# Kernel optimization log

Measured on AMD Instinct MI355X. Metric: run time of the kernel, lower is better.

## Reference

```python
import jax, jax.numpy as jnp
import numpy as np

B, HI, WI = 4, 24, 24
T = HI * WI
H, N = 12, 64
C = H * N
D_MIX, D_DECAY, D_AAA, D_KKK, D_GATE, D_MA, D_MK = 32, 64, 16, 16, 128, 16, 16


def q_shift(x, Hi, Wi):
    # 4-direction quarter-channel spatial shift (groups_q_shift, K=1, gamma=1/4)
    Bb, Nn, Cc = x.shape
    q = Cc // 4
    x4 = x.reshape(Bb, Hi, Wi, Cc)
    pad = lambda a, pw: jnp.pad(a, ((0, 0),) + pw + ((0, 0),))
    s1 = pad(x4[:, :, :-1, 0:q], ((0, 0), (1, 0)))        # shift right along W
    s2 = pad(x4[:, :, 1:, q:2 * q], ((0, 0), (0, 1)))     # shift left along W
    s3 = pad(x4[:, :-1, :, 2 * q:3 * q], ((1, 0), (0, 0)))  # shift down along H
    s4 = pad(x4[:, 1:, :, 3 * q:4 * q], ((0, 1), (0, 0)))   # shift up along H
    return jnp.concatenate([s1, s2, s3, s4], axis=-1).reshape(Bb, Nn, Cc)


def wkv7(r, w, k, v, a, b):
    # RWKV-7 delta-rule recurrence: S = S*diag(exp(w)) + S@(a b^T) + v k^T ; y = S r
    Bb, Tt, Cc = r.shape
    tohead = lambda t: t.reshape(Bb, Tt, H, N).transpose(1, 0, 2, 3)  # (T,B,H,N)
    rt, kt, vt, at, bt = map(tohead, (r, k, v, a, b))
    dt = jnp.exp(tohead(w))  # per-channel decay in (0, e^-0.5]

    def step(S, inp):
        r_, d_, k_, v_, a_, b_ = inp
        sa = jnp.einsum('bhij,bhj->bhi', S, a_)
        S = S * d_[:, :, None, :] + sa[..., None] * b_[:, :, None, :] + v_[..., None] * k_[:, :, None, :]
        return S, jnp.einsum('bhij,bhj->bhi', S, r_)

    S0 = jnp.zeros((Bb, H, N, N), r.dtype)
    _, ys = jax.lax.scan(step, S0, (rt, dt, kt, vt, at, bt))
    return ys.transpose(1, 0, 2, 3).reshape(Bb, Tt, Cc)


def group_norm(x, scale, bias, eps=64e-5):
    Bb, Tt, Cc = x.shape
    xg = x.reshape(Bb, Tt, H, N)
    mu = xg.mean(-1, keepdims=True)
    var = ((xg - mu) ** 2).mean(-1, keepdims=True)
    xn = ((xg - mu) * jax.lax.rsqrt(var + eps)).reshape(Bb, Tt, Cc)
    return xn * scale + bias


def fwd(x, maa_x, maa_rg, maa_wa, maa_k, maa_v, maa_w1, maa_w2,
        w0, wd1, wd2, a0, a1, a2, kk1, kk2, g1, g2,
        ma0, ma1, ma2, mk0, mk1, mk2, faaaa,
        Wr, Wk, Wv, Wo, ln_s, ln_b, h_img, w_img):
    Bb, Tt, Cc = x.shape
    xx = q_shift(x, h_img, w_img) - x
    xxx = x + xx * maa_x
    lora = jnp.tanh(xxx @ maa_w1).reshape(Bb, Tt, 4, D_MIX)
    m = jnp.einsum('btfd,fdc->fbtc', lora, maa_w2)  # (4,B,T,C)
    xrg = x + xx * (maa_rg + m[0])
    xwa = x + xx * (maa_wa + m[1])
    xk = x + xx * (maa_k + m[2])
    xv = x + xx * (maa_v + m[3])
    r = xrg @ Wr.T
    w = -jax.nn.softplus(-(w0 + jnp.tanh(xwa @ wd1) @ wd2)) - 0.5  # log-decay <= -0.5
    k = xk @ Wk.T
    v = xv @ Wv.T
    g = jax.nn.sigmoid(xrg @ g1) @ g2
    kk = k + jnp.tanh(xk @ kk1) @ kk2
    kkh = kk.reshape(Bb, Tt, H, N)
    kk = (kkh / jnp.maximum(jnp.linalg.norm(kkh, axis=-1, keepdims=True), 1e-12)).reshape(Bb, Tt, Cc)
    a = jax.nn.sigmoid(a0 + (xwa @ a1) @ a2)
    ma = jax.nn.sigmoid(ma0 + (xwa @ ma1) @ ma2)
    k = k * ma + k * a * (1.0 - ma)
    mk = jax.nn.sigmoid(mk0 + (xwa @ mk1) @ mk2)
    k = k * jnp.exp(jnp.minimum(w * mk, 0.0))
    y = wkv7(r, w, k, v, -kk, kk * a)
    y = group_norm(y, ln_s, ln_b)
    rh, kh, vh = (t.reshape(Bb, Tt, H, N) for t in (r, k, v))
    y = y + ((rh * kh * faaaa).sum(-1, keepdims=True) * vh).reshape(Bb, Tt, Cc)
    return (y * g) @ Wo.T


def setup_inputs() -> dict:
    key = jax.random.key(0)
    ks = iter(jax.random.split(key, 40))
    rn = lambda shape, s=0.02: jax.random.normal(next(ks), shape, jnp.float32) * s
    return {
        'x': rn((B, T, C), 1.0),
        'maa_x': rn((1, 1, C), 0.5), 'maa_rg': rn((1, 1, C), 0.5),
        'maa_wa': rn((1, 1, C), 0.5), 'maa_k': rn((1, 1, C), 0.5), 'maa_v': rn((1, 1, C), 0.5),
        'maa_w1': rn((C, 4 * D_MIX)), 'maa_w2': rn((4, D_MIX, C), 0.1),
        'w0': rn((1, 1, C), 0.5) - 4.0,
        'wd1': rn((C, D_DECAY)), 'wd2': rn((D_DECAY, C), 0.1),
        'a0': rn((1, 1, C), 0.1), 'a1': rn((C, D_AAA)), 'a2': rn((D_AAA, C), 0.1),
        'kk1': rn((C, D_KKK)), 'kk2': rn((D_KKK, C), 0.1),
        'g1': rn((C, D_GATE), 0.1), 'g2': rn((D_GATE, C), 0.1),
        'ma0': rn((1, 1, C), 0.1), 'ma1': rn((C, D_MA)), 'ma2': rn((D_MA, C), 0.1),
        'mk0': rn((1, 1, C), 0.1), 'mk1': rn((C, D_MK)), 'mk2': rn((D_MK, C), 0.1),
        'faaaa': rn((1, 1, H, N), 0.1),
        'Wr': rn((C, C)), 'Wk': rn((C, C)), 'Wv': rn((C, C)), 'Wo': rn((C, C)),
        'ln_s': jnp.ones((C,), jnp.float32), 'ln_b': jnp.zeros((C,), jnp.float32),
        'h_img': HI, 'w_img': WI,
    }


def reference(x, maa_x, maa_rg, maa_wa, maa_k, maa_v, maa_w1, maa_w2,
              w0, wd1, wd2, a0, a1, a2, kk1, kk2, g1, g2,
              ma0, ma1, ma2, mk0, mk1, mk2, faaaa,
              Wr, Wk, Wv, Wo, ln_s, ln_b, h_img, w_img):
    return fwd(x, maa_x, maa_rg, maa_wa, maa_k, maa_v, maa_w1, maa_w2,
               w0, wd1, wd2, a0, a1, a2, kk1, kk2, g1, g2,
               ma0, ma1, ma2, mk0, mk1, mk2, faaaa,
               Wr, Wk, Wv, Wo, ln_s, ln_b, h_img, w_img)
```

## Files before the change

### kernel.cpp

```cpp
#include <hip/hip_runtime.h>
#include <stdint.h>

#define Hh 12
#define Cc 768
#define Tt 576
#define BTC 1769472L
#define HI_ 24
#define WI_ 24
#define CH 16
#define NCH 36
#define RB 16
#define NRB 4

typedef unsigned int uint;
typedef unsigned short ushort;
typedef __attribute__((ext_vector_type(8))) short short8;
typedef __attribute__((ext_vector_type(4))) float f32x4;

__device__ __forceinline__ ushort f2b(float f) {
  uint u = __float_as_uint(f);
  u += 0x7FFFu + ((u >> 16) & 1u);
  return (ushort)(u >> 16);
}
__device__ __forceinline__ float b2f(ushort h) { return __uint_as_float(((uint)h) << 16); }
__device__ __forceinline__ float sigm(float x) { return 1.0f / (1.0f + __expf(-x)); }

__device__ __forceinline__ float dppx1(float x) {
  return __int_as_float(__builtin_amdgcn_mov_dpp(__float_as_int(x), 0xB1, 0xF, 0xF, true));
}
__device__ __forceinline__ float dppx2(float x) {
  return __int_as_float(__builtin_amdgcn_mov_dpp(__float_as_int(x), 0x4E, 0xF, 0xF, true));
}
__device__ __forceinline__ float mir8(float x) {
  return __int_as_float(__builtin_amdgcn_mov_dpp(__float_as_int(x), 0x141, 0xF, 0xF, true));
}

#define PUT2(buf, i, SZ, vexpr)                      \
  {                                                  \
    float _v = (vexpr);                              \
    ushort _h = f2b(_v);                             \
    (buf)[i] = _h;                                   \
    (buf)[(long)(SZ) + (i)] = f2b(_v - b2f(_h));     \
  }

__global__ __launch_bounds__(256) void gemm_hl(
    const ushort* __restrict__ Ah_, const ushort* __restrict__ Al_,
    const ushort* __restrict__ Bh_, const ushort* __restrict__ Bl_,
    float* __restrict__ C,
    int N, int K, int lda, int ldb, int ldc, long sA, long sB, long sC) {
  Ah_ += (long)blockIdx.z * sA;
  Al_ += (long)blockIdx.z * sA;
  Bh_ += (long)blockIdx.z * sB;
  Bl_ += (long)blockIdx.z * sB;
  C += (long)blockIdx.z * sC;
  __shared__ ushort sAh[64][40], sAl[64][40], sBh[64][40], sBl[64][40];
  const int bm = blockIdx.x * 64, bn = blockIdx.y * 64;
  const int tid = threadIdx.x;
  const int wave = tid >> 6, lane = tid & 63;
  const int wm = (wave >> 1) * 32, wn = (wave & 1) * 32;
  const int srow = tid >> 2, scol = (tid & 3) * 8;
  const int fr = lane & 15, kg = (lane >> 4) * 8;
  f32x4 acc[2][2] = {};
  const int bnrow = bn + srow;
  const bool bok = bnrow < N;
  const ushort* aph = Ah_ + (long)(bm + srow) * lda + scol;
  const ushort* apl = Al_ + (long)(bm + srow) * lda + scol;
  const ushort* bph = Bh_ + (long)bnrow * ldb + scol;
  const ushort* bpl = Bl_ + (long)bnrow * ldb + scol;
  for (int k0 = 0; k0 < K; k0 += 32) {
    short8 avh = *(const short8*)(aph + k0);
    short8 avl = *(const short8*)(apl + k0);
    short8 bvh = {0, 0, 0, 0, 0, 0, 0, 0}, bvl = {0, 0, 0, 0, 0, 0, 0, 0};
    if (bok) { bvh = *(const short8*)(bph + k0); bvl = *(const short8*)(bpl + k0); }
    __syncthreads();
    *(short8*)&sAh[srow][scol] = avh;
    *(short8*)&sAl[srow][scol] = avl;
    *(short8*)&sBh[srow][scol] = bvh;
    *(short8*)&sBl[srow][scol] = bvl;
    __syncthreads();
    short8 bfh[2], bfl[2];
#pragma unroll
    for (int ni = 0; ni < 2; ni++) {
      bfh[ni] = *(const short8*)&sBh[wn + ni * 16 + fr][kg];
      bfl[ni] = *(const short8*)&sBl[wn + ni * 16 + fr][kg];
    }
#pragma unroll
    for (int mi = 0; mi < 2; mi++) {
      short8 afh = *(const short8*)&sAh[wm + mi * 16 + fr][kg];
      short8 afl = *(const short8*)&sAl[wm + mi * 16 + fr][kg];
#pragma unroll
      for (int ni = 0; ni < 2; ni++) {
        acc[mi][ni] = __builtin_amdgcn_mfma_f32_16x16x32_bf16(afh, bfh[ni], acc[mi][ni], 0, 0, 0);
        acc[mi][ni] = __builtin_amdgcn_mfma_f32_16x16x32_bf16(afh, bfl[ni], acc[mi][ni], 0, 0, 0);
        acc[mi][ni] = __builtin_amdgcn_mfma_f32_16x16x32_bf16(afl, bfh[ni], acc[mi][ni], 0, 0, 0);
      }
    }
  }
  const int row4 = (lane >> 4) * 4;
#pragma unroll
  for (int mi = 0; mi < 2; mi++)
#pragma unroll
    for (int ni = 0; ni < 2; ni++) {
      int gc = bn + wn + ni * 16 + fr;
      if (gc < N) {
        long base = (long)(bm + wm + mi * 16 + row4) * ldc + gc;
#pragma unroll
        for (int rr = 0; rr < 4; rr++) C[base + (long)rr * ldc] = acc[mi][ni][rr];
      }
    }
}

__global__ __launch_bounds__(256) void gemm_hl3(
    const ushort* __restrict__ Ah_, const ushort* __restrict__ Al_,
    const ushort* __restrict__ Bh_, const ushort* __restrict__ Bl_,
    float* __restrict__ C,
    int K, int lda, int ldb, int ldc, long sA, long sB, long sC) {
  Ah_ += (long)blockIdx.z * sA;
  Al_ += (long)blockIdx.z * sA;
  Bh_ += (long)blockIdx.z * sB;
  Bl_ += (long)blockIdx.z * sB;
  C += (long)blockIdx.z * sC;
  __shared__ ushort sAh[128][40], sAl[128][40], sBh[64][40], sBl[64][40];
  const int bm = blockIdx.x * 128, bn = blockIdx.y * 64;
  const int tid = threadIdx.x;
  const int wave = tid >> 6, lane = tid & 63;
  const int wm = (wave >> 1) * 64, wn = (wave & 1) * 32;
  const int srow = tid >> 2, scol = (tid & 3) * 8;
  const int fr = lane & 15, kg = (lane >> 4) * 8;
  f32x4 acc[4][2] = {};
  const ushort* aph = Ah_ + (long)(bm + srow) * lda + scol;
  const ushort* apl = Al_ + (long)(bm + srow) * lda + scol;
  const ushort* bph = Bh_ + (long)(bn + srow) * ldb + scol;
  const ushort* bpl = Bl_ + (long)(bn + srow) * ldb + scol;
  const long a64 = 64L * lda;
  for (int k0 = 0; k0 < K; k0 += 32) {
    short8 avh0 = *(const short8*)(aph + k0);
    short8 avh1 = *(const short8*)(aph + a64 + k0);
    short8 avl0 = *(const short8*)(apl + k0);
    short8 avl1 = *(const short8*)(apl + a64 + k0);
    short8 bvh0 = *(const short8*)(bph + k0);
    short8 bvl0 = *(const short8*)(bpl + k0);
    __syncthreads();
    *(short8*)&sAh[srow][scol] = avh0;
    *(short8*)&sAh[srow + 64][scol] = avh1;
    *(short8*)&sAl[srow][scol] = avl0;
    *(short8*)&sAl[srow + 64][scol] = avl1;
    *(short8*)&sBh[srow][scol] = bvh0;
    *(short8*)&sBl[srow][scol] = bvl0;
    __syncthreads();
    short8 bfh[2], bfl[2];
#pragma unroll
    for (int ni = 0; ni < 2; ni++) {
      bfh[ni] = *(const short8*)&sBh[wn + ni * 16 + fr][kg];
      bfl[ni] = *(const short8*)&sBl[wn + ni * 16 + fr][kg];
    }
#pragma unroll
    for (int mi = 0; mi < 4; mi++) {
      short8 afh = *(const short8*)&sAh[wm + mi * 16 + fr][kg];
      short8 afl = *(const short8*)&sAl[wm + mi * 16 + fr][kg];
#pragma unroll
      for (int ni = 0; ni < 2; ni++) {
        acc[mi][ni] = __builtin_amdgcn_mfma_f32_16x16x32_bf16(afh, bfh[ni], acc[mi][ni], 0, 0, 0);
        acc[mi][ni] = __builtin_amdgcn_mfma_f32_16x16x32_bf16(afh, bfl[ni], acc[mi][ni], 0, 0, 0);
        acc[mi][ni] = __builtin_amdgcn_mfma_f32_16x16x32_bf16(afl, bfh[ni], acc[mi][ni], 0, 0, 0);
      }
    }
  }
  const int row4 = (lane >> 4) * 4;
#pragma unroll
  for (int mi = 0; mi < 4; mi++)
#pragma unroll
    for (int ni = 0; ni < 2; ni++) {
      int gc = bn + wn + ni * 16 + fr;
      long base = (long)(bm + wm + mi * 16 + row4) * ldc + gc;
#pragma unroll
      for (int rr = 0; rr < 4; rr++) C[base + (long)rr * ldc] = acc[mi][ni][rr];
    }
}

__global__ __launch_bounds__(256) void conv_bigw(const float* __restrict__ Wr,
                                                 const float* __restrict__ Wk,
                                                 const float* __restrict__ Wv,
                                                 const float* __restrict__ Wo,
                                                 ushort* __restrict__ Wb) {
  long idx = (long)blockIdx.x * 256 + threadIdx.x;
  const long WSZ = 589824;
  int seg = (int)(idx / WSZ);
  long off = idx % WSZ;
  const float* s = (seg == 0) ? Wr : (seg == 1) ? Wk : (seg == 2) ? Wv : Wo;
  PUT2(Wb, idx, 2359296L, s[off]);
}

__global__ __launch_bounds__(256) void prep_smallw(
    const float* maa_w1, const float* maa_w2, const float* wd1, const float* wd2,
    const float* a1, const float* a2, const float* kk1, const float* kk2,
    const float* g1, const float* g2, const float* ma1, const float* ma2,
    const float* mk1, const float* mk2, ushort* w1T, ushort* w2T, ushort* wcat1,
    ushort* kk1T, ushort* g1T, ushort* wd2T, ushort* armk2T, ushort* g2T) {
  int idx = blockIdx.x * 256 + threadIdx.x;
  if (idx < 98304) { int n = idx / 768, c = idx % 768; PUT2(w1T, idx, 98304, maa_w1[c * 128 + n]); return; }
  idx -= 98304;
  if (idx < 98304) {
    int f = idx / 24576, r = idx % 24576; int n = r / 32, d = r % 32;
    PUT2(w2T, idx, 98304, maa_w2[(f * 32 + d) * 768 + n]); return;
  }
  idx -= 98304;
  if (idx < 49152) { int n = idx / 768, c = idx % 768; PUT2(wcat1, idx, 86016, wd1[c * 64 + n]); return; }
  idx -= 49152;
  if (idx < 12288) { int n = idx / 768, c = idx % 768; PUT2(wcat1, 49152 + idx, 86016, a1[c * 16 + n]); return; }
  idx -= 12288;
  if (idx < 12288) { int n = idx / 768, c = idx % 768; PUT2(wcat1, 61440 + idx, 86016, ma1[c * 16 + n]); return; }
  idx -= 12288;
  if (idx < 12288) { int n = idx / 768, c = idx % 768; PUT2(wcat1, 73728 + idx, 86016, mk1[c * 16 + n]); return; }
  idx -= 12288;
  if (idx < 12288) { int n = idx / 768, c = idx % 768; PUT2(kk1T, idx, 12288, kk1[c * 16 + n]); return; }
  idx -= 12288;
  if (idx < 98304) { int n = idx / 768, c = idx % 768; PUT2(g1T, idx, 98304, g1[c * 128 + n]); return; }
  idx -= 98304;
  if (idx < 49152) { int n = idx / 64, d = idx % 64; PUT2(wd2T, idx, 49152, wd2[d * 768 + n]); return; }
  idx -= 49152;
  if (idx < 98304) {
    int f = idx / 24576, r = idx % 24576; int n = r / 32, d = r % 32;
    const float* s = (f == 0) ? a2 : (f == 1) ? ma2 : (f == 2) ? mk2 : kk2;
    float v = (d < 16) ? s[d * 768 + n] : 0.0f;
    PUT2(armk2T, idx, 98304, v); return;
  }
  idx -= 98304;
  if (idx < 98304) { int n = idx / 128, d = idx % 128; PUT2(g2T, idx, 98304, g2[d * 768 + n]); }
}

__global__ __launch_bounds__(256) void qshift_mix(const float* __restrict__ x,
                                                  const float* __restrict__ maa_x,
                                                  float* __restrict__ xx,
                                                  ushort* __restrict__ xxxs) {
  long idx = (long)blockIdx.x * 256 + threadIdx.x;
  int c = (int)(idx % Cc);
  int bt = (int)(idx / Cc);
  int t = bt % Tt;
  int hh = t / WI_, ww = t % WI_;
  int q = c / 192;
  float s = 0.f;
  if (q == 0) { if (ww > 0) s = x[idx - Cc]; }
  else if (q == 1) { if (ww < WI_ - 1) s = x[idx + Cc]; }
  else if (q == 2) { if (hh > 0) s = x[idx - (long)WI_ * Cc]; }
  else { if (hh < HI_ - 1) s = x[idx + (long)WI_ * Cc]; }
  float xv = x[idx];
  float d = s - xv;
  xx[idx] = d;
  PUT2(xxxs, idx, BTC, xv + d * maa_x[c]);
}

__global__ __launch_bounds__(256) void tanh_split(const float* __restrict__ in,
                                                  ushort* __restrict__ out) {
  int i = blockIdx.x * 256 + threadIdx.x;
  PUT2(out, i, 294912, tanhf(in[i]));
}

__global__ __launch_bounds__(256) void mix4(const float* __restrict__ x,
                                            const float* __restrict__ xx,
                                            const float* __restrict__ m,
                                            const float* __restrict__ maa_rg,
                                            const float* __restrict__ maa_wa,
                                            const float* __restrict__ maa_k,
                                            const float* __restrict__ maa_v,
                                            ushort* __restrict__ x4s) {
  long idx = (long)blockIdx.x * 256 + threadIdx.x;
  int c = (int)(idx % Cc);
  float xv = x[idx], d = xx[idx];
  PUT2(x4s, idx, 4 * BTC, xv + d * (maa_rg[c] + m[idx]));
  PUT2(x4s, idx + BTC, 4 * BTC, xv + d * (maa_k[c] + m[idx + 2 * BTC]));
  PUT2(x4s, idx + 2 * BTC, 4 * BTC, xv + d * (maa_v[c] + m[idx + 3 * BTC]));
  PUT2(x4s, idx + 3 * BTC, 4 * BTC, xv + d * (maa_wa[c] + m[idx + BTC]));
}

__global__ __launch_bounds__(256) void build_a2(const float* __restrict__ wlora,
                                                const float* __restrict__ kklora,
                                                const float* __restrict__ glora,
                                                ushort* __restrict__ A2s,
                                                ushort* __restrict__ glss) {
  int idx = blockIdx.x * 256 + threadIdx.x;
  const int NA2 = 2304 * 160;
  if (idx < NA2) {
    int bt = idx / 160, col = idx % 160;
    float v;
    if (col < 64) v = tanhf(wlora[bt * 112 + col]);
    else if (col < 112) v = wlora[bt * 112 + col];
    else if (col < 128) v = tanhf(kklora[bt * 16 + (col - 112)]);
    else v = 0.0f;
    PUT2(A2s, idx, 368640, v);
    return;
  }
  idx -= NA2;
  PUT2(glss, idx, 294912, sigm(glora[idx]));
}

__global__ __launch_bounds__(256) void post_rwkv(
    const float* __restrict__ k, const float* __restrict__ wraw, const float* __restrict__ w0,
    const float* __restrict__ a0, const float* __restrict__ ma0, const float* __restrict__ mk0,
    float* araw, float* maraw, float* mkraw, float* kkraw) {
  int gw = blockIdx.x * 4 + (threadIdx.x >> 6);
  int j = threadIdx.x & 63;
  int bt = gw / Hh, h = gw % Hh;
  int c = h * 64 + j;
  long idx = (long)bt * Cc + c;
  float kv = k[idx];
  float kkv = kv + kkraw[idx];
  float ss = kkv * kkv;
  for (int mm = 1; mm < 64; mm <<= 1) ss += __shfl_xor(ss, mm, 64);
  float rn = 1.0f / fmaxf(sqrtf(ss), 1e-12f);
  float kkn = kkv * rn;
  float z = w0[c] + wraw[idx];
  float w = fminf(z, 0.f) - log1pf(__expf(-fabsf(z))) - 0.5f;
  float a = sigm(a0[c] + araw[idx]);
  float ma = sigm(ma0[c] + maraw[idx]);
  float mk = sigm(mk0[c] + mkraw[idx]);
  float k2 = kv * ma + kv * a * (1.f - ma);
  float k3 = k2 * __expf(fminf(w * mk, 0.f));
  araw[idx] = -kkn;
  maraw[idx] = kkn * a;
  mkraw[idx] = __expf(w);
  kkraw[idx] = k3;
}

__global__ __launch_bounds__(128, 1) void wkv7(const float* __restrict__ r,
                                               const float* __restrict__ dd,
                                               const float* __restrict__ kk,
                                               const float* __restrict__ vv,
                                               const float* __restrict__ aa,
                                               const float* __restrict__ bb,
                                               float* __restrict__ y) {
  __shared__ float sc[2][5][CH][64];
  __shared__ float sv[2][CH][RB];
  const int blk = blockIdx.x;
  const int bh = blk >> 2;
  const int rb = blk & 3;
  const int b = bh / Hh, h = bh % Hh;
  const int tid = threadIdx.x;
  const int wave = tid >> 6, lane = tid & 63;
  const int rl = lane >> 3, cg = lane & 7;
  const int row = rb * RB + wave * 8 + rl;
  const int cb = cg * 8;
  const int vri = wave * 8 + rl;
  const long vecbase = ((long)b * Tt) * Cc + h * 64;
  float* py = y + vecbase + row;
  const float* gp[5] = {r, dd, kk, aa, bb};
  float S[8];
#pragma unroll
  for (int u = 0; u < 8; u++) S[u] = 0.f;
  f32x4 gq[10];
  float gv[2];
  f32x4 Xq[10], Yq[10];
  float Xv, Yv;

#define SLOAD(t0)                                                              \
  {                                                                            \
    _Pragma("unroll") for (int q = 0; q < 10; q++) {                           \
      const int arr = q >> 1;                                                  \
      const int i2 = ((q & 1) << 7) + tid;                                     \
      gq[q] = *(const f32x4*)(gp[arr] + vecbase + (long)((t0) + (i2 >> 4)) * Cc \
                              + ((i2 & 15) << 2));                             \
    }                                                                          \
    _Pragma("unroll") for (int j = 0; j < 2; j++) {                            \
      const int i2 = (j << 7) + tid;                                           \
      gv[j] = vv[vecbase + (long)((t0) + (i2 >> 4)) * Cc + rb * RB + (i2 & 15)]; \
    }                                                                          \
  }
#define SWRITE(bi)                                                             \
  {                                                                            \
    _Pragma("unroll") for (int q = 0; q < 10; q++) {                           \
      const int i2 = ((q & 1) << 7) + tid;                                     \
      *(f32x4*)&sc[bi][q >> 1][i2 >> 4][(i2 & 15) << 2] = gq[q];               \
    }                                                                          \
    _Pragma("unroll") for (int j = 0; j < 2; j++) {                            \
      const int i2 = (j << 7) + tid;                                           \
      sv[bi][i2 >> 4][i2 & 15] = gv[j];                                        \
    }                                                                          \
  }
#define LREAD(Q, Vv_, pb, t)                                                   \
  {                                                                            \
    Q[0] = *(const f32x4*)&sc[pb][3][t][cb];                                   \
    Q[1] = *(const f32x4*)&sc[pb][3][t][cb + 4];                               \
    Q[2] = *(const f32x4*)&sc[pb][1][t][cb];                                   \
    Q[3] = *(const f32x4*)&sc[pb][1][t][cb + 4];                               \
    Q[4] = *(const f32x4*)&sc[pb][2][t][cb];                                   \
    Q[5] = *(const f32x4*)&sc[pb][2][t][cb + 4];                               \
    Q[6] = *(const f32x4*)&sc[pb][4][t][cb];                                   \
    Q[7] = *(const f32x4*)&sc[pb][4][t][cb + 4];                               \
    Q[8] = *(const f32x4*)&sc[pb][0][t][cb];                                   \
    Q[9] = *(const f32x4*)&sc[pb][0][t][cb + 4];                               \
    Vv_ = sv[pb][t][vri];                                                      \
  }
#define WCOMP(Q, Vv_, yoff)                                                    \
  {                                                                            \
    float p0 = S[0] * Q[0][0] + S[4] * Q[1][0];                                \
    float p1 = S[1] * Q[0][1] + S[5] * Q[1][1];                                \
    float p2 = S[2] * Q[0][2] + S[6] * Q[1][2];                                \
    float p3 = S[3] * Q[0][3] + S[7] * Q[1][3];                                \
    float sa = (p0 + p1) + (p2 + p3);                                          \
    sa += dppx1(sa); sa += dppx2(sa); sa += mir8(sa);                          \
    float q0, q1, q2, q3;                                                      \
    S[0] = fmaf(S[0], Q[2][0], fmaf(sa, Q[6][0], Vv_ * Q[4][0])); q0 = S[0] * Q[8][0]; \
    S[1] = fmaf(S[1], Q[2][1], fmaf(sa, Q[6][1], Vv_ * Q[4][1])); q1 = S[1] * Q[8][1]; \
    S[2] = fmaf(S[2], Q[2][2], fmaf(sa, Q[6][2], Vv_ * Q[4][2])); q2 = S[2] * Q[8][2]; \
    S[3] = fmaf(S[3], Q[2][3], fmaf(sa, Q[6][3], Vv_ * Q[4][3])); q3 = S[3] * Q[8][3]; \
    S[4] = fmaf(S[4], Q[3][0], fmaf(sa, Q[7][0], Vv_ * Q[5][0])); q0 += S[4] * Q[9][0]; \
    S[5] = fmaf(S[5], Q[3][1], fmaf(sa, Q[7][1], Vv_ * Q[5][1])); q1 += S[5] * Q[9][1]; \
    S[6] = fmaf(S[6], Q[3][2], fmaf(sa, Q[7][2], Vv_ * Q[5][2])); q2 += S[6] * Q[9][2]; \
    S[7] = fmaf(S[7], Q[3][3], fmaf(sa, Q[7][3], Vv_ * Q[5][3])); q3 += S[7] * Q[9][3]; \
    float yp = (q0 + q1) + (q2 + q3);                                          \
    yp += dppx1(yp); yp += dppx2(yp); yp += mir8(yp);                          \
    if (cg == 0) py[yoff] = yp;                                                \
  }

  SLOAD(0);
  SWRITE(0);
  __syncthreads();
  SLOAD(CH);
  for (int ch = 0; ch < NCH; ch++) {
    const int pb = ch & 1;
    const long ybase = (long)ch * CH * Cc;
    LREAD(Xq, Xv, pb, 0);
#pragma unroll
    for (int t = 0; t < CH; t += 2) {
      LREAD(Yq, Yv, pb, t + 1);
      WCOMP(Xq, Xv, ybase + (long)t * Cc);
      if (t + 2 < CH) LREAD(Xq, Xv, pb, t + 2);
      WCOMP(Yq, Yv, ybase + (long)(t + 1) * Cc);
    }
    __syncthreads();
    if (ch + 1 < NCH) {
      SWRITE(pb ^ 1);
      if (ch + 2 < NCH) SLOAD((ch + 2) * CH);
    }
    __syncthreads();
  }
#undef SLOAD
#undef SWRITE
#undef LREAD
#undef WCOMP
}

__global__ __launch_bounds__(256) void gn_bonus_gate(
    const float* __restrict__ y, const float* __restrict__ r, const float* __restrict__ k3,
    const float* __restrict__ v, const float* __restrict__ g, const float* __restrict__ faaaa,
    const float* __restrict__ lns, const float* __restrict__ lnb, ushort* __restrict__ ygs) {
  int gw = blockIdx.x * 4 + (threadIdx.x >> 6);
  int j = threadIdx.x & 63;
  int bt = gw / Hh, h = gw % Hh;
  int c = h * 64 + j;
  long idx = (long)bt * Cc + c;
  float yv = y[idx];
  float s1 = yv, s2 = yv * yv;
  float s3 = r[idx] * k3[idx] * faaaa[c];
  for (int mm = 1; mm < 64; mm <<= 1) {
    s1 += __shfl_xor(s1, mm, 64);
    s2 += __shfl_xor(s2, mm, 64);
    s3 += __shfl_xor(s3, mm, 64);
  }
  float mu = s1 * (1.f / 64.f);
  float var = s2 * (1.f / 64.f) - mu * mu;
  float xn = (yv - mu) * rsqrtf(var + 64e-5f);
  float y2 = xn * lns[c] + lnb[c] + s3 * v[idx];
  PUT2(ygs, idx, BTC, y2 * g[idx]);
}

extern "C" void kernel_launch(void* const* d_in, const int* in_sizes, int n_in,
                              void* d_out, int out_size, void* d_ws, size_t ws_size,
                              hipStream_t stream) {
  const float* x = (const float*)d_in[0];
  const float* maa_x = (const float*)d_in[1];
  const float* maa_rg = (const float*)d_in[2];
  const float* maa_wa = (const float*)d_in[3];
  const float* maa_k = (const float*)d_in[4];
  const float* maa_v = (const float*)d_in[5];
  const float* maa_w1 = (const float*)d_in[6];
  const float* maa_w2 = (const float*)d_in[7];
  const float* w0 = (const float*)d_in[8];
  const float* wd1 = (const float*)d_in[9];
  const float* wd2 = (const float*)d_in[10];
  const float* a0 = (const float*)d_in[11];
  const float* a1 = (const float*)d_in[12];
  const float* a2 = (const float*)d_in[13];
  const float* kk1 = (const float*)d_in[14];
  const float* kk2 = (const float*)d_in[15];
  const float* g1 = (const float*)d_in[16];
  const float* g2 = (const float*)d_in[17];
  const float* ma0 = (const float*)d_in[18];
  const float* ma1 = (const float*)d_in[19];
  const float* ma2 = (const float*)d_in[20];
  const float* mk0 = (const float*)d_in[21];
  const float* mk1 = (const float*)d_in[22];
  const float* mk2 = (const float*)d_in[23];
  const float* faaaa = (const float*)d_in[24];
  const float* Wr = (const float*)d_in[25];
  const float* Wk = (const float*)d_in[26];
  const float* Wv = (const float*)d_in[27];
  const float* Wo = (const float*)d_in[28];
  const float* lns = (const float*)d_in[29];
  const float* lnb = (const float*)d_in[30];

  float* fw = (float*)d_ws;
  float* xx = fw;
  float* m = fw + BTC;
  float* rbuf = fw + 5 * BTC;
  float* kbuf = fw + 6 * BTC;
  float* vbuf = fw + 7 * BTC;
  float* wrawb = fw + 8 * BTC;
  float* gbuf = fw + 9 * BTC;
  float* ybuf = fw + 10 * BTC;
  float* lora_raw = fw + 11 * BTC;
  float* wlora = lora_raw + 294912;
  float* glora = wlora + 258048;
  float* kklora = glora + 294912;
  ushort* ub = (ushort*)(fw + 11 * BTC + 884736);
  ushort* xxxs = ub;   ub += 2 * BTC;
  ushort* x4s = ub;    ub += 8 * BTC;
  ushort* lts = ub;    ub += 2 * 294912;
  ushort* A2s = ub;    ub += 2 * 368640;
  ushort* glss = ub;   ub += 2 * 294912;
  ushort* ygs = ub;    ub += 2 * BTC;
  ushort* Wb = ub;     ub += 2 * 2359296L;
  ushort* w1T = ub;    ub += 2 * 98304;
  ushort* w2T = ub;    ub += 2 * 98304;
  ushort* wcat1 = ub;  ub += 2 * 86016;
  ushort* kk1T = ub;   ub += 2 * 12288;
  ushort* g1T = ub;    ub += 2 * 98304;
  ushort* wd2T = ub;   ub += 2 * 49152;
  ushort* armk2T = ub; ub += 2 * 98304;
  ushort* g2T = ub;    ub += 2 * 98304;

  dim3 blk(256);
  conv_bigw<<<9216, blk, 0, stream>>>(Wr, Wk, Wv, Wo, Wb);
  prep_smallw<<<2496, blk, 0, stream>>>(maa_w1, maa_w2, wd1, wd2, a1, a2, kk1, kk2, g1, g2,
                                        ma1, ma2, mk1, mk2, w1T, w2T, wcat1, kk1T, g1T, wd2T,
                                        armk2T, g2T);
  qshift_mix<<<6912, blk, 0, stream>>>(x, maa_x, xx, xxxs);
  gemm_hl3<<<dim3(18, 2, 1), blk, 0, stream>>>(xxxs, xxxs + BTC, w1T, w1T + 98304, lora_raw,
                                               768, 768, 768, 128, 0, 0, 0);
  tanh_split<<<1152, blk, 0, stream>>>(lora_raw, lts);
  gemm_hl3<<<dim3(18, 12, 4), blk, 0, stream>>>(lts, lts + 294912, w2T, w2T + 98304, m,
                                                32, 128, 32, 768, 32, 24576, BTC);
  mix4<<<6912, blk, 0, stream>>>(x, xx, m, maa_rg, maa_wa, maa_k, maa_v, x4s);
  gemm_hl3<<<dim3(18, 12, 3), blk, 0, stream>>>(x4s, x4s + 4 * BTC, Wb, Wb + 2359296L, rbuf,
                                                768, 768, 768, 768, BTC, 589824, BTC);
  gemm_hl<<<dim3(36, 2, 1), blk, 0, stream>>>(x4s + 3 * BTC, x4s + 7 * BTC, wcat1, wcat1 + 86016,
                                              wlora, 112, 768, 768, 768, 112, 0, 0, 0);
  gemm_hl3<<<dim3(18, 2, 1), blk, 0, stream>>>(x4s, x4s + 4 * BTC, g1T, g1T + 98304, glora,
                                               768, 768, 768, 128, 0, 0, 0);
  gemm_hl<<<dim3(36, 1, 1), blk, 0, stream>>>(x4s + BTC, x4s + 5 * BTC, kk1T, kk1T + 12288,
                                              kklora, 16, 768, 768, 768, 16, 0, 0, 0);
  build_a2<<<2592, blk, 0, stream>>>(wlora, kklora, glora, A2s, glss);
  gemm_hl3<<<dim3(18, 12, 1), blk, 0, stream>>>(A2s, A2s + 368640, wd2T, wd2T + 49152, wrawb,
                                                64, 160, 64, 768, 0, 0, 0);
  gemm_hl3<<<dim3(18, 12, 4), blk, 0, stream>>>(A2s + 64, A2s + 368640 + 64, armk2T,
                                                armk2T + 98304, m, 32, 160, 32, 768,
                                                16, 24576, BTC);
  gemm_hl3<<<dim3(18, 12, 1), blk, 0, stream>>>(glss, glss + 294912, g2T, g2T + 98304, gbuf,
                                                128, 128, 128, 768, 0, 0, 0);
  post_rwkv<<<6912, blk, 0, stream>>>(kbuf, wrawb, w0, a0, ma0, mk0,
                                      m, m + BTC, m + 2 * BTC, m + 3 * BTC);
  wkv7<<<192, dim3(128), 0, stream>>>(rbuf, m + 2 * BTC, m + 3 * BTC, vbuf, m, m + BTC, ybuf);
  gn_bonus_gate<<<6912, blk, 0, stream>>>(ybuf, rbuf, m + 3 * BTC, vbuf, gbuf, faaaa,
                                          lns, lnb, ygs);
  gemm_hl3<<<dim3(18, 12, 1), blk, 0, stream>>>(ygs, ygs + BTC, Wb + 3L * 589824,
                                                Wb + 2359296L + 3L * 589824, (float*)d_out,
                                                768, 768, 768, 768, 0, 0, 0);
}
```

Measured before the change: 449.0 us.

## Group GEMMs into multi-segment launches with fused tanh/sigmoid/mix epilogues

Replaces the separate gemm_hl/gemm_hl3 launches with a single gemm_multi kernel. Each launch takes a table of up to six GEMM segments and picks its segment from the block index, so the independent projections share one launch and fill more CUs. Elementwise steps are folded into GEMM epilogues: tanh for the first LoRA, the mix4 interpolation for the second, and sigmoid for the gate LoRA. This removes the tanh_split and mix4 kernels and their fp32 round trips. Small-N weights are zero-padded to 64-column tiles so all segments use the 128x64 tile. The cost is per-block segment selection, runtime epilogue branching, and some wasted work on the padding.

New measurement: 395.0 us. 12.0% less time.

```diff
diff --git a/kernel.cpp b/kernel.cpp
--- a/kernel.cpp
+++ b/kernel.cpp
@@ -10,7 +10,6 @@
 #define CH 16
 #define NCH 36
 #define RB 16
-#define NRB 4
 
 typedef unsigned int uint;
 typedef unsigned short ushort;
@@ -43,97 +42,42 @@
     (buf)[(long)(SZ) + (i)] = f2b(_v - b2f(_h));     \
   }
 
-__global__ __launch_bounds__(256) void gemm_hl(
-    const ushort* __restrict__ Ah_, const ushort* __restrict__ Al_,
-    const ushort* __restrict__ Bh_, const ushort* __restrict__ Bl_,
-    float* __restrict__ C,
-    int N, int K, int lda, int ldb, int ldc, long sA, long sB, long sC) {
-  Ah_ += (long)blockIdx.z * sA;
-  Al_ += (long)blockIdx.z * sA;
-  Bh_ += (long)blockIdx.z * sB;
-  Bl_ += (long)blockIdx.z * sB;
-  C += (long)blockIdx.z * sC;
-  __shared__ ushort sAh[64][40], sAl[64][40], sBh[64][40], sBl[64][40];
-  const int bm = blockIdx.x * 64, bn = blockIdx.y * 64;
-  const int tid = threadIdx.x;
-  const int wave = tid >> 6, lane = tid & 63;
-  const int wm = (wave >> 1) * 32, wn = (wave & 1) * 32;
-  const int srow = tid >> 2, scol = (tid & 3) * 8;
-  const int fr = lane & 15, kg = (lane >> 4) * 8;
-  f32x4 acc[2][2] = {};
-  const int bnrow = bn + srow;
-  const bool bok = bnrow < N;
-  const ushort* aph = Ah_ + (long)(bm + srow) * lda + scol;
-  const ushort* apl = Al_ + (long)(bm + srow) * lda + scol;
-  const ushort* bph = Bh_ + (long)bnrow * ldb + scol;
-  const ushort* bpl = Bl_ + (long)bnrow * ldb + scol;
-  for (int k0 = 0; k0 < K; k0 += 32) {
-    short8 avh = *(const short8*)(aph + k0);
-    short8 avl = *(const short8*)(apl + k0);
-    short8 bvh = {0, 0, 0, 0, 0, 0, 0, 0}, bvl = {0, 0, 0, 0, 0, 0, 0, 0};
-    if (bok) { bvh = *(const short8*)(bph + k0); bvl = *(const short8*)(bpl + k0); }
-    __syncthreads();
-    *(short8*)&sAh[srow][scol] = avh;
-    *(short8*)&sAl[srow][scol] = avl;
-    *(short8*)&sBh[srow][scol] = bvh;
-    *(short8*)&sBl[srow][scol] = bvl;
-    __syncthreads();
-    short8 bfh[2], bfl[2];
-#pragma unroll
-    for (int ni = 0; ni < 2; ni++) {
-      bfh[ni] = *(const short8*)&sBh[wn + ni * 16 + fr][kg];
-      bfl[ni] = *(const short8*)&sBl[wn + ni * 16 + fr][kg];
-    }
-#pragma unroll
-    for (int mi = 0; mi < 2; mi++) {
-      short8 afh = *(const short8*)&sAh[wm + mi * 16 + fr][kg];
-      short8 afl = *(const short8*)&sAl[wm + mi * 16 + fr][kg];
-#pragma unroll
-      for (int ni = 0; ni < 2; ni++) {
-        acc[mi][ni] = __builtin_amdgcn_mfma_f32_16x16x32_bf16(afh, bfh[ni], acc[mi][ni], 0, 0, 0);
-        acc[mi][ni] = __builtin_amdgcn_mfma_f32_16x16x32_bf16(afh, bfl[ni], acc[mi][ni], 0, 0, 0);
-        acc[mi][ni] = __builtin_amdgcn_mfma_f32_16x16x32_bf16(afl, bfh[ni], acc[mi][ni], 0, 0, 0);
-      }
-    }
-  }
-  const int row4 = (lane >> 4) * 4;
-#pragma unroll
-  for (int mi = 0; mi < 2; mi++)
-#pragma unroll
-    for (int ni = 0; ni < 2; ni++) {
-      int gc = bn + wn + ni * 16 + fr;
-      if (gc < N) {
-        long base = (long)(bm + wm + mi * 16 + row4) * ldc + gc;
-#pragma unroll
-        for (int rr = 0; rr < 4; rr++) C[base + (long)rr * ldc] = acc[mi][ni][rr];
-      }
-    }
-}
-
-__global__ __launch_bounds__(256) void gemm_hl3(
-    const ushort* __restrict__ Ah_, const ushort* __restrict__ Al_,
-    const ushort* __restrict__ Bh_, const ushort* __restrict__ Bl_,
-    float* __restrict__ C,
-    int K, int lda, int ldb, int ldc, long sA, long sB, long sC) {
-  Ah_ += (long)blockIdx.z * sA;
-  Al_ += (long)blockIdx.z * sA;
-  Bh_ += (long)blockIdx.z * sB;
-  Bl_ += (long)blockIdx.z * sB;
-  C += (long)blockIdx.z * sC;
+struct Seg {
+  const ushort* Ah; const ushort* Al; const ushort* Bh; const ushort* Bl;
+  float* C; ushort* O; const float* maap;
+  long osz;
+  int K, lda, ldb, ldc, nby, epi;
+};
+struct SegPack {
+  Seg s[6];
+  int cum[6];
+  const float* x; const float* xx;
+};
+
+__global__ __launch_bounds__(256) void gemm_multi(SegPack P) {
   __shared__ ushort sAh[128][40], sAl[128][40], sBh[64][40], sBl[64][40];
-  const int bm = blockIdx.x * 128, bn = blockIdx.y * 64;
+  const int bid = blockIdx.x;
+  int si = 0;
+#pragma unroll
+  for (int i = 1; i < 6; i++) si = (bid >= P.cum[i]) ? i : si;
+  const Seg sg = P.s[si];
+  const int local = bid - P.cum[si];
+  const int bx = local / sg.nby;
+  const int by = local - bx * sg.nby;
+  const int bm = bx * 128, bn = by * 64;
   const int tid = threadIdx.x;
   const int wave = tid >> 6, lane = tid & 63;
   const int wm = (wave >> 1) * 64, wn = (wave & 1) * 32;
   const int srow = tid >> 2, scol = (tid & 3) * 8;
   const int fr = lane & 15, kg = (lane >> 4) * 8;
   f32x4 acc[4][2] = {};
-  const ushort* aph = Ah_ + (long)(bm + srow) * lda + scol;
-  const ushort* apl = Al_ + (long)(bm + srow) * lda + scol;
-  const ushort* bph = Bh_ + (long)(bn + srow) * ldb + scol;
-  const ushort* bpl = Bl_ + (long)(bn + srow) * ldb + scol;
+  const int lda = sg.lda, ldb = sg.ldb;
+  const ushort* aph = sg.Ah + (long)(bm + srow) * lda + scol;
+  const ushort* apl = sg.Al + (long)(bm + srow) * lda + scol;
+  const ushort* bph = sg.Bh + (long)(bn + srow) * ldb + scol;
+  const ushort* bpl = sg.Bl + (long)(bn + srow) * ldb + scol;
   const long a64 = 64L * lda;
-  for (int k0 = 0; k0 < K; k0 += 32) {
+  for (int k0 = 0; k0 < sg.K; k0 += 32) {
     short8 avh0 = *(const short8*)(aph + k0);
     short8 avh1 = *(const short8*)(aph + a64 + k0);
     short8 avl0 = *(const short8*)(apl + k0);
@@ -167,15 +111,48 @@
     }
   }
   const int row4 = (lane >> 4) * 4;
-#pragma unroll
-  for (int mi = 0; mi < 4; mi++)
-#pragma unroll
-    for (int ni = 0; ni < 2; ni++) {
-      int gc = bn + wn + ni * 16 + fr;
-      long base = (long)(bm + wm + mi * 16 + row4) * ldc + gc;
-#pragma unroll
-      for (int rr = 0; rr < 4; rr++) C[base + (long)rr * ldc] = acc[mi][ni][rr];
-    }
+  const int ldc = sg.ldc;
+  if (sg.epi == 0) {
+#pragma unroll
+    for (int mi = 0; mi < 4; mi++)
+#pragma unroll
+      for (int ni = 0; ni < 2; ni++) {
+        int gc = bn + wn + ni * 16 + fr;
+        long base = (long)(bm + wm + mi * 16 + row4) * ldc + gc;
+#pragma unroll
+        for (int rr = 0; rr < 4; rr++) sg.C[base + (long)rr * ldc] = acc[mi][ni][rr];
+      }
+  } else if (sg.epi == 3) {
+#pragma unroll
+    for (int mi = 0; mi < 4; mi++)
+#pragma unroll
+      for (int ni = 0; ni < 2; ni++) {
+        int gc = bn + wn + ni * 16 + fr;
+        long base = (long)(bm + wm + mi * 16 + row4) * 768 + gc;
+        float mc = sg.maap[gc];
+#pragma unroll
+        for (int rr = 0; rr < 4; rr++) {
+          long ix = base + (long)rr * 768;
+          float xv = P.x[ix], d = P.xx[ix];
+          PUT2(sg.O, ix, sg.osz, xv + d * (mc + acc[mi][ni][rr]));
+        }
+      }
+  } else {
+    const bool istanh = (sg.epi == 1);
+#pragma unroll
+    for (int mi = 0; mi < 4; mi++)
+#pragma unroll
+      for (int ni = 0; ni < 2; ni++) {
+        int gc = bn + wn + ni * 16 + fr;
+        long base = (long)(bm + wm + mi * 16 + row4) * ldc + gc;
+#pragma unroll
+        for (int rr = 0; rr < 4; rr++) {
+          float v = acc[mi][ni][rr];
+          v = istanh ? tanhf(v) : sigm(v);
+          PUT2(sg.O, base + (long)rr * ldc, sg.osz, v);
+        }
+      }
+  }
 }
 
 __global__ __launch_bounds__(256) void conv_bigw(const float* __restrict__ Wr,
@@ -205,16 +182,20 @@
     PUT2(w2T, idx, 98304, maa_w2[(f * 32 + d) * 768 + n]); return;
   }
   idx -= 98304;
-  if (idx < 49152) { int n = idx / 768, c = idx % 768; PUT2(wcat1, idx, 86016, wd1[c * 64 + n]); return; }
+  if (idx < 49152) { int n = idx / 768, c = idx % 768; PUT2(wcat1, idx, 98304, wd1[c * 64 + n]); return; }
   idx -= 49152;
-  if (idx < 12288) { int n = idx / 768, c = idx % 768; PUT2(wcat1, 49152 + idx, 86016, a1[c * 16 + n]); return; }
+  if (idx < 12288) { int n = idx / 768, c = idx % 768; PUT2(wcat1, 49152 + idx, 98304, a1[c * 16 + n]); return; }
   idx -= 12288;
-  if (idx < 12288) { int n = idx / 768, c = idx % 768; PUT2(wcat1, 61440 + idx, 86016, ma1[c * 16 + n]); return; }
+  if (idx < 12288) { int n = idx / 768, c = idx % 768; PUT2(wcat1, 61440 + idx, 98304, ma1[c * 16 + n]); return; }
   idx -= 12288;
-  if (idx < 12288) { int n = idx / 768, c = idx % 768; PUT2(wcat1, 73728 + idx, 86016, mk1[c * 16 + n]); return; }
+  if (idx < 12288) { int n = idx / 768, c = idx % 768; PUT2(wcat1, 73728 + idx, 98304, mk1[c * 16 + n]); return; }
   idx -= 12288;
-  if (idx < 12288) { int n = idx / 768, c = idx % 768; PUT2(kk1T, idx, 12288, kk1[c * 16 + n]); return; }
+  if (idx < 12288) { wcat1[86016 + idx] = 0; wcat1[98304 + 86016 + idx] = 0; return; }
   idx -= 12288;
+  if (idx < 12288) { int n = idx / 768, c = idx % 768; PUT2(kk1T, idx, 49152, kk1[c * 16 + n]); return; }
+  idx -= 12288;
+  if (idx < 36864) { kk1T[12288 + idx] = 0; kk1T[49152 + 12288 + idx] = 0; return; }
+  idx -= 36864;
   if (idx < 98304) { int n = idx / 768, c = idx % 768; PUT2(g1T, idx, 98304, g1[c * 128 + n]); return; }
   idx -= 98304;
   if (idx < 49152) { int n = idx / 64, d = idx % 64; PUT2(wd2T, idx, 49152, wd2[d * 768 + n]); return; }
@@ -250,48 +231,17 @@
   PUT2(xxxs, idx, BTC, xv + d * maa_x[c]);
 }
 
-__global__ __launch_bounds__(256) void tanh_split(const float* __restrict__ in,
-                                                  ushort* __restrict__ out) {
-  int i = blockIdx.x * 256 + threadIdx.x;
-  PUT2(out, i, 294912, tanhf(in[i]));
-}
-
-__global__ __launch_bounds__(256) void mix4(const float* __restrict__ x,
-                                            const float* __restrict__ xx,
-                                            const float* __restrict__ m,
-                                            const float* __restrict__ maa_rg,
-                                            const float* __restrict__ maa_wa,
-                                            const float* __restrict__ maa_k,
-                                            const float* __restrict__ maa_v,
-                                            ushort* __restrict__ x4s) {
-  long idx = (long)blockIdx.x * 256 + threadIdx.x;
-  int c = (int)(idx % Cc);
-  float xv = x[idx], d = xx[idx];
-  PUT2(x4s, idx, 4 * BTC, xv + d * (maa_rg[c] + m[idx]));
-  PUT2(x4s, idx + BTC, 4 * BTC, xv + d * (maa_k[c] + m[idx + 2 * BTC]));
-  PUT2(x4s, idx + 2 * BTC, 4 * BTC, xv + d * (maa_v[c] + m[idx + 3 * BTC]));
-  PUT2(x4s, idx + 3 * BTC, 4 * BTC, xv + d * (maa_wa[c] + m[idx + BTC]));
-}
-
 __global__ __launch_bounds__(256) void build_a2(const float* __restrict__ wlora,
                                                 const float* __restrict__ kklora,
-                                                const float* __restrict__ glora,
-                                                ushort* __restrict__ A2s,
-                                                ushort* __restrict__ glss) {
+                                                ushort* __restrict__ A2s) {
   int idx = blockIdx.x * 256 + threadIdx.x;
-  const int NA2 = 2304 * 160;
-  if (idx < NA2) {
-    int bt = idx / 160, col = idx % 160;
-    float v;
-    if (col < 64) v = tanhf(wlora[bt * 112 + col]);
-    else if (col < 112) v = wlora[bt * 112 + col];
-    else if (col < 128) v = tanhf(kklora[bt * 16 + (col - 112)]);
-    else v = 0.0f;
-    PUT2(A2s, idx, 368640, v);
-    return;
-  }
-  idx -= NA2;
-  PUT2(glss, idx, 294912, sigm(glora[idx]));
+  int bt = idx / 160, col = idx % 160;
+  float v;
+  if (col < 64) v = tanhf(wlora[bt * 128 + col]);
+  else if (col < 112) v = wlora[bt * 128 + col];
+  else if (col < 128) v = tanhf(kklora[bt * 64 + (col - 112)]);
+  else v = 0.0f;
+  PUT2(A2s, idx, 368640, v);
 }
 
 __global__ __launch_bounds__(256) void post_rwkv(
@@ -508,11 +458,9 @@
   float* wrawb = fw + 8 * BTC;
   float* gbuf = fw + 9 * BTC;
   float* ybuf = fw + 10 * BTC;
-  float* lora_raw = fw + 11 * BTC;
-  float* wlora = lora_raw + 294912;
-  float* glora = wlora + 258048;
-  float* kklora = glora + 294912;
-  ushort* ub = (ushort*)(fw + 11 * BTC + 884736);
+  float* wlora = fw + 11 * BTC;
+  float* kklora = wlora + 294912;
+  ushort* ub = (ushort*)(kklora + 147456);
   ushort* xxxs = ub;   ub += 2 * BTC;
   ushort* x4s = ub;    ub += 8 * BTC;
   ushort* lts = ub;    ub += 2 * 294912;
@@ -522,47 +470,95 @@
   ushort* Wb = ub;     ub += 2 * 2359296L;
   ushort* w1T = ub;    ub += 2 * 98304;
   ushort* w2T = ub;    ub += 2 * 98304;
-  ushort* wcat1 = ub;  ub += 2 * 86016;
-  ushort* kk1T = ub;   ub += 2 * 12288;
+  ushort* wcat1 = ub;  ub += 2 * 98304;
+  ushort* kk1T = ub;   ub += 2 * 49152;
   ushort* g1T = ub;    ub += 2 * 98304;
   ushort* wd2T = ub;   ub += 2 * 49152;
   ushort* armk2T = ub; ub += 2 * 98304;
   ushort* g2T = ub;    ub += 2 * 98304;
 
+  const int IMAX = 0x7fffffff;
   dim3 blk(256);
   conv_bigw<<<9216, blk, 0, stream>>>(Wr, Wk, Wv, Wo, Wb);
-  prep_smallw<<<2496, blk, 0, stream>>>(maa_w1, maa_w2, wd1, wd2, a1, a2, kk1, kk2, g1, g2,
+  prep_smallw<<<2688, blk, 0, stream>>>(maa_w1, maa_w2, wd1, wd2, a1, a2, kk1, kk2, g1, g2,
                                         ma1, ma2, mk1, mk2, w1T, w2T, wcat1, kk1T, g1T, wd2T,
                                         armk2T, g2T);
   qshift_mix<<<6912, blk, 0, stream>>>(x, maa_x, xx, xxxs);
-  gemm_hl3<<<dim3(18, 2, 1), blk, 0, stream>>>(xxxs, xxxs + BTC, w1T, w1T + 98304, lora_raw,
-                                               768, 768, 768, 128, 0, 0, 0);
-  tanh_split<<<1152, blk, 0, stream>>>(lora_raw, lts);
-  gemm_hl3<<<dim3(18, 12, 4), blk, 0, stream>>>(lts, lts + 294912, w2T, w2T + 98304, m,
-                                                32, 128, 32, 768, 32, 24576, BTC);
-  mix4<<<6912, blk, 0, stream>>>(x, xx, m, maa_rg, maa_wa, maa_k, maa_v, x4s);
-  gemm_hl3<<<dim3(18, 12, 3), blk, 0, stream>>>(x4s, x4s + 4 * BTC, Wb, Wb + 2359296L, rbuf,
-                                                768, 768, 768, 768, BTC, 589824, BTC);
-  gemm_hl<<<dim3(36, 2, 1), blk, 0, stream>>>(x4s + 3 * BTC, x4s + 7 * BTC, wcat1, wcat1 + 86016,
-                                              wlora, 112, 768, 768, 768, 112, 0, 0, 0);
-  gemm_hl3<<<dim3(18, 2, 1), blk, 0, stream>>>(x4s, x4s + 4 * BTC, g1T, g1T + 98304, glora,
-                                               768, 768, 768, 128, 0, 0, 0);
-  gemm_hl<<<dim3(36, 1, 1), blk, 0, stream>>>(x4s + BTC, x4s + 5 * BTC, kk1T, kk1T + 12288,
-                                              kklora, 16, 768, 768, 768, 16, 0, 0, 0);
-  build_a2<<<2592, blk, 0, stream>>>(wlora, kklora, glora, A2s, glss);
-  gemm_hl3<<<dim3(18, 12, 1), blk, 0, stream>>>(A2s, A2s + 368640, wd2T, wd2T + 49152, wrawb,
-                                                64, 160, 64, 768, 0, 0, 0);
-  gemm_hl3<<<dim3(18, 12, 4), blk, 0, stream>>>(A2s + 64, A2s + 368640 + 64, armk2T,
-                                                armk2T + 98304, m, 32, 160, 32, 768,
-                                                16, 24576, BTC);
-  gemm_hl3<<<dim3(18, 12, 1), blk, 0, stream>>>(glss, glss + 294912, g2T, g2T + 98304, gbuf,
-                                                128, 128, 128, 768, 0, 0, 0);
+
+  {
+    SegPack P = {};
+    P.s[0] = {xxxs, xxxs + BTC, w1T, w1T + 98304, nullptr, lts, nullptr,
+              294912, 768, 768, 768, 128, 2, 1};
+    P.cum[0] = 0;
+    for (int i = 1; i < 6; i++) P.cum[i] = IMAX;
+    P.x = x; P.xx = xx;
+    gemm_multi<<<36, blk, 0, stream>>>(P);
+  }
+  {
+    SegPack P = {};
+    const float* maaps[4] = {maa_rg, maa_wa, maa_k, maa_v};
+    const int planes[4] = {0, 3, 1, 2};
+    for (int f = 0; f < 4; f++) {
+      P.s[f] = {lts + f * 32, lts + 294912 + f * 32, w2T + f * 24576,
+                w2T + 98304 + f * 24576, nullptr, x4s + (long)planes[f] * BTC, maaps[f],
+                4 * BTC, 32, 128, 32, 768, 12, 3};
+      P.cum[f] = f * 216;
+    }
+    for (int i = 4; i < 6; i++) P.cum[i] = IMAX;
+    P.x = x; P.xx = xx;
+    gemm_multi<<<864, blk, 0, stream>>>(P);
+  }
+  {
+    SegPack P = {};
+    for (int f = 0; f < 3; f++) {
+      float* cout = (f == 0) ? rbuf : (f == 1) ? kbuf : vbuf;
+      P.s[f] = {x4s + (long)f * BTC, x4s + (long)(4 + f) * BTC, Wb + (long)f * 589824,
+                Wb + 2359296L + (long)f * 589824, cout, nullptr, nullptr,
+                0, 768, 768, 768, 768, 12, 0};
+      P.cum[f] = f * 216;
+    }
+    P.s[3] = {x4s + 3 * BTC, x4s + 7 * BTC, wcat1, wcat1 + 98304, wlora, nullptr, nullptr,
+              0, 768, 768, 768, 128, 2, 0};
+    P.cum[3] = 648;
+    P.s[4] = {x4s, x4s + 4 * BTC, g1T, g1T + 98304, nullptr, glss, nullptr,
+              294912, 768, 768, 768, 128, 2, 2};
+    P.cum[4] = 684;
+    P.s[5] = {x4s + BTC, x4s + 5 * BTC, kk1T, kk1T + 49152, kklora, nullptr, nullptr,
+              0, 768, 768, 768, 64, 1, 0};
+    P.cum[5] = 720;
+    P.x = x; P.xx = xx;
+    gemm_multi<<<738, blk, 0, stream>>>(P);
+  }
+  build_a2<<<1440, blk, 0, stream>>>(wlora, kklora, A2s);
+  {
+    SegPack P = {};
+    P.s[0] = {A2s, A2s + 368640, wd2T, wd2T + 49152, wrawb, nullptr, nullptr,
+              0, 64, 160, 64, 768, 12, 0};
+    P.cum[0] = 0;
+    for (int f = 0; f < 4; f++) {
+      P.s[1 + f] = {A2s + 64 + 16 * f, A2s + 368640 + 64 + 16 * f, armk2T + f * 24576,
+                    armk2T + 98304 + f * 24576, m + (long)f * BTC, nullptr, nullptr,
+                    0, 32, 160, 32, 768, 12, 0};
+      P.cum[1 + f] = 216 + f * 216;
+    }
+    P.s[5] = {glss, glss + 294912, g2T, g2T + 98304, gbuf, nullptr, nullptr,
+              0, 128, 128, 128, 768, 12, 0};
+    P.cum[5] = 1080;
+    P.x = x; P.xx = xx;
+    gemm_multi<<<1296, blk, 0, stream>>>(P);
+  }
   post_rwkv<<<6912, blk, 0, stream>>>(kbuf, wrawb, w0, a0, ma0, mk0,
                                       m, m + BTC, m + 2 * BTC, m + 3 * BTC);
   wkv7<<<192, dim3(128), 0, stream>>>(rbuf, m + 2 * BTC, m + 3 * BTC, vbuf, m, m + BTC, ybuf);
   gn_bonus_gate<<<6912, blk, 0, stream>>>(ybuf, rbuf, m + 3 * BTC, vbuf, gbuf, faaaa,
                                           lns, lnb, ygs);
-  gemm_hl3<<<dim3(18, 12, 1), blk, 0, stream>>>(ygs, ygs + BTC, Wb + 3L * 589824,
-                                                Wb + 2359296L + 3L * 589824, (float*)d_out,
-                                                768, 768, 768, 768, 0, 0, 0);
-}
+  {
+    SegPack P = {};
+    P.s[0] = {ygs, ygs + BTC, Wb + 3L * 589824, Wb + 2359296L + 3L * 589824,
+              (float*)d_out, nullptr, nullptr, 0, 768, 768, 768, 768, 12, 0};
+    P.cum[0] = 0;
+    for (int i = 1; i < 6; i++) P.cum[i] = IMAX;
+    P.x = x; P.xx = xx;
+    gemm_multi<<<216, blk, 0, stream>>>(P);
+  }
+}
```
